# Optimization experiments

Hardware: AMD Instinct MI355X
Metric: run time of the kernel (lower is better)

The kernel has to match this reference:

```python
import jax, jax.numpy as jnp
import numpy as np

N_NODES = 500000
N_EDGES = 8000000
N_FIELDS = 4
GRAD_LIMIT = 30000.0
EPS = 1e-8


def setup_inputs() -> dict:
    key = jax.random.key(0)
    k1, k2, k3 = jax.random.split(key, 3)
    pos = jax.random.normal(k1, (N_NODES, 2), dtype=jnp.float32)
    edge_index = jax.random.randint(k2, (2, N_EDGES), 0, N_NODES, dtype=jnp.int32)
    field = jax.random.normal(k3, (N_NODES, N_FIELDS), dtype=jnp.float32)
    return {"pos": pos, "edge_index": edge_index, "field": field}


def reference(pos, edge_index, field):
    # pos: [N,2], edge_index: [2,E] int, field: [N,F]
    row, col = edge_index[0], edge_index[1]
    N = pos.shape[0]

    # Per-edge position differences (detached in the original -> stop_gradient)
    dX = jax.lax.stop_gradient(pos[col] - pos[row])  # [E,2]

    # Outer products and scatter-add into per-node 2x2 moment matrices
    M_edge = dX[:, :, None] * dX[:, None, :]                     # [E,2,2]
    M_node = jax.ops.segment_sum(M_edge, row, num_segments=N)    # [N,2,2]
    M_node = M_node + EPS * jnp.eye(2, dtype=jnp.float32)
    M_inv = jnp.linalg.inv(M_node)                               # [N,2,2]

    # All field variables at once (original loops over columns; math identical)
    du = field[col] - field[row]                                 # [E,F]
    V_edge = dX[:, :, None] * du[:, None, :]                     # [E,2,F]
    V_node = jax.ops.segment_sum(V_edge, row, num_segments=N)    # [N,2,F]

    grads = jnp.einsum('nij,njf->nif', M_inv, V_node)            # [N,2,F]
    grads = jnp.clip(grads, -GRAD_LIMIT, GRAD_LIMIT)
    # Original returns a list of F arrays of shape [N,2]; stack as [F,N,2]
    return jnp.transpose(grads, (2, 0, 1)).astype(pos.dtype)
```

## Files before the change

### kernel.cpp

```cpp
#include <hip/hip_runtime.h>
#include <hip/hip_bf16.h>


#define GRAD_LIMIT 30000.0f
#define EPS 1e-8

#define NBUCKET_MAX 1024
#define BSHIFT 9
#define BSIZE 512
#define CHUNK 8192
#define BTHREADS 512
#define PER_THREAD (CHUNK / BTHREADS)
#define CAP 10240

__global__ void pack_kernel(const float2* __restrict__ pos,
                            const float4* __restrict__ field,
                            float4* __restrict__ packed, int N) {
    int n = blockIdx.x * blockDim.x + threadIdx.x;
    if (n >= N) return;
    float2 p = pos[n];
    float4 f = field[n];
    packed[2 * n + 0] = make_float4(p.x, p.y, f.x, f.y);
    packed[2 * n + 1] = make_float4(f.z, f.w, 0.f, 0.f);
}

__global__ void __launch_bounds__(BTHREADS)
bucket_count_kernel(const int* __restrict__ rows, int* __restrict__ bucket_cnt,
                    int E, int nbuckets) {
    __shared__ int hist[NBUCKET_MAX];
    for (int i = threadIdx.x; i < nbuckets; i += blockDim.x) hist[i] = 0;
    __syncthreads();

    int base = blockIdx.x * CHUNK;
    int lim = E - base;
    if (lim > CHUNK) lim = CHUNK;
    for (int k = threadIdx.x; k < lim; k += blockDim.x) {
        int r = rows[base + k];
        atomicAdd(&hist[r >> BSHIFT], 1);
    }
    __syncthreads();
    for (int i = threadIdx.x; i < nbuckets; i += blockDim.x) {
        int c = hist[i];
        if (c) atomicAdd(&bucket_cnt[i], c);
    }
}

__global__ void bucket_scan_kernel(const int* __restrict__ bucket_cnt,
                                   int* __restrict__ bucket_start,
                                   int* __restrict__ cursor, int nb) {
    __shared__ int s[NBUCKET_MAX];
    int t = threadIdx.x;
    int v = (t < nb) ? bucket_cnt[t] : 0;
    s[t] = v;
    __syncthreads();
    for (int d = 1; d < NBUCKET_MAX; d <<= 1) {
        int x = (t >= d) ? s[t - d] : 0;
        __syncthreads();
        s[t] += x;
        __syncthreads();
    }
    if (t < nb) {
        int ex = s[t] - v;
        bucket_start[t] = ex;
        cursor[t] = ex;
    }
}

__global__ void __launch_bounds__(BTHREADS)
bucket_scatter_kernel(const int* __restrict__ rows, const int* __restrict__ cols,
                      int* __restrict__ cursor, unsigned* __restrict__ payload,
                      int E, int nbuckets) {
    __shared__ int hist[NBUCKET_MAX];
    __shared__ int lbase[NBUCKET_MAX];
    for (int i = threadIdx.x; i < nbuckets; i += blockDim.x) hist[i] = 0;
    __syncthreads();

    int base = blockIdx.x * CHUNK;
    int lim = E - base;
    if (lim > CHUNK) lim = CHUNK;

    unsigned pk[PER_THREAD];
    int bl[PER_THREAD];
#pragma unroll
    for (int k = 0; k < PER_THREAD; ++k) {
        int idx = k * BTHREADS + threadIdx.x;
        if (idx < lim) {
            int e = base + idx;
            int r = rows[e];
            int c = cols[e];
            int b = r >> BSHIFT;
            int lr = atomicAdd(&hist[b], 1);
            pk[k] = ((unsigned)(r & (BSIZE - 1)) << 19) | (unsigned)c;
            bl[k] = (b << 13) | lr;
        } else {
            bl[k] = -1;
        }
    }
    __syncthreads();
    for (int i = threadIdx.x; i < nbuckets; i += blockDim.x) {
        int c = hist[i];
        lbase[i] = c ? atomicAdd(&cursor[i], c) : 0;
    }
    __syncthreads();
#pragma unroll
    for (int k = 0; k < PER_THREAD; ++k) {
        if (bl[k] >= 0) {
            int b = bl[k] >> 13;
            int lr = bl[k] & 8191;
            payload[lbase[b] + lr] = pk[k];
        }
    }
}

__global__ void __launch_bounds__(BSIZE)
bucket_sort_accum_solve(const float4* __restrict__ packed,
                        const int* __restrict__ bucket_start,
                        const int* __restrict__ cursor,
                        const unsigned* __restrict__ payload,
                        float* __restrict__ out,
                        int N) {
    __shared__ unsigned sorted[CAP];
    __shared__ int hist[BSIZE];
    __shared__ int incl[BSIZE];
    __shared__ int cur[BSIZE];

    int t = threadIdx.x;
    int b = blockIdx.x;
    int node0 = b << BSHIFT;

    float4 ra = make_float4(0.f, 0.f, 0.f, 0.f);
    float4 rb = ra;
    if (node0 + t < N) {
        ra = packed[2 * (node0 + t) + 0];
        rb = packed[2 * (node0 + t) + 1];
    }

    float m00 = 0.f, m01 = 0.f, m11 = 0.f;
    float v00 = 0.f, v01 = 0.f, v02 = 0.f, v03 = 0.f;
    float v10 = 0.f, v11 = 0.f, v12 = 0.f, v13 = 0.f;

    int s0 = bucket_start[b];
    int s1 = cursor[b];

    for (int cstart = s0; cstart < s1; cstart += CAP) {
        int cnt = s1 - cstart;
        if (cnt > CAP) cnt = CAP;

        hist[t] = 0;
        __syncthreads();

        for (int i = t; i < cnt; i += BSIZE) {
            unsigned p = payload[cstart + i];
            atomicAdd(&hist[p >> 19], 1);
        }
        __syncthreads();

        incl[t] = hist[t];
        __syncthreads();
        for (int d = 1; d < BSIZE; d <<= 1) {
            int x = (t >= d) ? incl[t - d] : 0;
            __syncthreads();
            incl[t] += x;
            __syncthreads();
        }
        cur[t] = incl[t] - hist[t];
        __syncthreads();

        for (int i = t; i < cnt; i += BSIZE) {
            unsigned p = payload[cstart + i];
            int k = atomicAdd(&cur[p >> 19], 1);
            sorted[k] = p;
        }
        __syncthreads();

        int st = incl[t] - hist[t];
        int en = incl[t];
        for (int k = st; k < en; ++k) {
            unsigned p = sorted[k];
            int c = (int)(p & 0x7FFFFu);
            float4 ca = packed[2 * c + 0];
            float4 cb = packed[2 * c + 1];
            float dx0 = ca.x - ra.x;
            float dx1 = ca.y - ra.y;
            float du0 = ca.z - ra.z;
            float du1 = ca.w - ra.w;
            float du2 = cb.x - rb.x;
            float du3 = cb.y - rb.y;
            m00 = fmaf(dx0, dx0, m00);
            m01 = fmaf(dx0, dx1, m01);
            m11 = fmaf(dx1, dx1, m11);
            v00 = fmaf(dx0, du0, v00);
            v01 = fmaf(dx0, du1, v01);
            v02 = fmaf(dx0, du2, v02);
            v03 = fmaf(dx0, du3, v03);
            v10 = fmaf(dx1, du0, v10);
            v11 = fmaf(dx1, du1, v11);
            v12 = fmaf(dx1, du2, v12);
            v13 = fmaf(dx1, du3, v13);
        }
        __syncthreads();
    }

    int n = node0 + t;
    if (n >= N) return;
    double M00 = (double)m00 + EPS;
    double M01 = (double)m01;
    double M11 = (double)m11 + EPS;
    double inv_det = 1.0 / (M00 * M11 - M01 * M01);
    double i00 = M11 * inv_det;
    double i01 = -M01 * inv_det;
    double i11 = M00 * inv_det;

    const float vf0[4] = {v00, v01, v02, v03};
    const float vf1[4] = {v10, v11, v12, v13};
#pragma unroll
    for (int f = 0; f < 4; ++f) {
        float ga = (float)(i00 * (double)vf0[f] + i01 * (double)vf1[f]);
        float gb = (float)(i01 * (double)vf0[f] + i11 * (double)vf1[f]);
        float2 o;
        o.x = fminf(fmaxf(ga, -GRAD_LIMIT), GRAD_LIMIT);
        o.y = fminf(fmaxf(gb, -GRAD_LIMIT), GRAD_LIMIT);
        *reinterpret_cast<float2*>(out + (size_t)f * N * 2 + (size_t)n * 2) = o;
    }
}

extern "C" void kernel_launch(void* const* d_in, const int* in_sizes, int n_in,
                              void* d_out, int out_size, void* d_ws, size_t ws_size,
                              hipStream_t stream) {
    const float2* pos = (const float2*)d_in[0];
    const int* edge_index = (const int*)d_in[1];
    const float4* field = (const float4*)d_in[2];
    float* out = (float*)d_out;

    const int N = in_sizes[0] / 2;
    const int E = in_sizes[1] / 2;

    const int* rows = edge_index;
    const int* cols = edge_index + E;

    const int nbuckets = (N + BSIZE - 1) / BSIZE;
    const int nblocksE = (E + CHUNK - 1) / CHUNK;

    float4* packed = (float4*)d_ws;
    int* bucket_cnt = (int*)(packed + (size_t)2 * N);
    int* bucket_start = bucket_cnt + NBUCKET_MAX;
    int* cursor = bucket_start + NBUCKET_MAX;
    unsigned* payload = (unsigned*)(cursor + NBUCKET_MAX);

    hipMemsetAsync(bucket_cnt, 0, NBUCKET_MAX * sizeof(int), stream);
    pack_kernel<<<(N + 255) / 256, 256, 0, stream>>>(pos, field, packed, N);
    bucket_count_kernel<<<nblocksE, BTHREADS, 0, stream>>>(rows, bucket_cnt, E,
                                                           nbuckets);
    bucket_scan_kernel<<<1, NBUCKET_MAX, 0, stream>>>(bucket_cnt, bucket_start,
                                                      cursor, nbuckets);
    bucket_scatter_kernel<<<nblocksE, BTHREADS, 0, stream>>>(rows, cols, cursor,
                                                             payload, E, nbuckets);
    bucket_sort_accum_solve<<<nbuckets, BSIZE, 0, stream>>>(packed, bucket_start,
                                                            cursor, payload,
                                                            out, N);
}
```

Measured before the change: 340.6 us.

## Replace atomic bucket cursors with per-block histogram scan and register-cached payload

Edge bucketing now writes a per-block bucket histogram matrix, column-scans it and scans the bucket totals. Each scatter block then gets fixed output offsets without global atomics or a staged register pass. The sort/accumulate kernel keeps its payload entries in registers between the histogram and placement passes, so it reads payload from global memory once instead of twice. CAP shrinks to 8192, which is close to the average edges per bucket, so many buckets may need a second small chunk pass with extra barriers.

```diff
diff --git a/kernel.cpp b/kernel.cpp
--- a/kernel.cpp
+++ b/kernel.cpp
@@ -11,7 +11,9 @@
 #define CHUNK 8192
 #define BTHREADS 512
 #define PER_THREAD (CHUNK / BTHREADS)
-#define CAP 10240
+#define CHUNK_E 16384
+#define CAP 8192
+#define KC_ITERS (CAP / BSIZE)
 
 __global__ void pack_kernel(const float2* __restrict__ pos,
                             const float4* __restrict__ field,
@@ -24,20 +26,98 @@
     packed[2 * n + 1] = make_float4(f.z, f.w, 0.f, 0.f);
 }
 
+
+__global__ void __launch_bounds__(BTHREADS)
+count2_kernel(const int* __restrict__ rows, int* __restrict__ counts,
+              int E, int nbuckets) {
+    __shared__ int hist[NBUCKET_MAX];
+    for (int i = threadIdx.x; i < nbuckets; i += blockDim.x) hist[i] = 0;
+    __syncthreads();
+    int base = blockIdx.x * CHUNK_E;
+    int lim = E - base;
+    if (lim > CHUNK_E) lim = CHUNK_E;
+    for (int k = threadIdx.x; k < lim; k += blockDim.x)
+        atomicAdd(&hist[rows[base + k] >> BSHIFT], 1);
+    __syncthreads();
+    int* row = counts + (size_t)blockIdx.x * nbuckets;
+    for (int i = threadIdx.x; i < nbuckets; i += blockDim.x) row[i] = hist[i];
+}
+
+__global__ void __launch_bounds__(512)
+colscan_kernel(int* __restrict__ counts, int* __restrict__ totals,
+               int nblk, int nbuckets) {
+    __shared__ int s[512];
+    int b = blockIdx.x;
+    int t = threadIdx.x;
+    int v = (t < nblk) ? counts[(size_t)t * nbuckets + b] : 0;
+    s[t] = v;
+    __syncthreads();
+    for (int d = 1; d < 512; d <<= 1) {
+        int x = (t >= d) ? s[t - d] : 0;
+        __syncthreads();
+        s[t] += x;
+        __syncthreads();
+    }
+    if (t < nblk) counts[(size_t)t * nbuckets + b] = s[t] - v;
+    if (t == 511) totals[b] = s[511];
+}
+
+__global__ void totscan_kernel(const int* __restrict__ totals,
+                               int* __restrict__ bucket_start, int nb) {
+    __shared__ int s[1024];
+    int t = threadIdx.x;
+    int v = (t < nb) ? totals[t] : 0;
+    s[t] = v;
+    __syncthreads();
+    for (int d = 1; d < 1024; d <<= 1) {
+        int x = (t >= d) ? s[t - d] : 0;
+        __syncthreads();
+        s[t] += x;
+        __syncthreads();
+    }
+    if (t < nb) bucket_start[t] = s[t] - v;
+}
+
+__global__ void __launch_bounds__(BTHREADS)
+scatter2_kernel(const int* __restrict__ rows, const int* __restrict__ cols,
+                const int* __restrict__ bucket_start,
+                const int* __restrict__ counts,
+                unsigned* __restrict__ payload, int E, int nbuckets) {
+    __shared__ int rank[NBUCKET_MAX];
+    __shared__ int lbase[NBUCKET_MAX];
+    int blk = blockIdx.x;
+    const int* pre = counts + (size_t)blk * nbuckets;
+    for (int i = threadIdx.x; i < nbuckets; i += blockDim.x) {
+        rank[i] = 0;
+        lbase[i] = bucket_start[i] + pre[i];
+    }
+    __syncthreads();
+    int base = blk * CHUNK_E;
+    int lim = E - base;
+    if (lim > CHUNK_E) lim = CHUNK_E;
+    for (int k = threadIdx.x; k < lim; k += blockDim.x) {
+        int e = base + k;
+        int r = rows[e];
+        int c = cols[e];
+        int b = r >> BSHIFT;
+        int lr = atomicAdd(&rank[b], 1);
+        payload[lbase[b] + lr] =
+            ((unsigned)(r & (BSIZE - 1)) << 19) | (unsigned)c;
+    }
+}
+
+
 __global__ void __launch_bounds__(BTHREADS)
 bucket_count_kernel(const int* __restrict__ rows, int* __restrict__ bucket_cnt,
                     int E, int nbuckets) {
     __shared__ int hist[NBUCKET_MAX];
     for (int i = threadIdx.x; i < nbuckets; i += blockDim.x) hist[i] = 0;
     __syncthreads();
-
     int base = blockIdx.x * CHUNK;
     int lim = E - base;
     if (lim > CHUNK) lim = CHUNK;
-    for (int k = threadIdx.x; k < lim; k += blockDim.x) {
-        int r = rows[base + k];
-        atomicAdd(&hist[r >> BSHIFT], 1);
-    }
+    for (int k = threadIdx.x; k < lim; k += blockDim.x)
+        atomicAdd(&hist[rows[base + k] >> BSHIFT], 1);
     __syncthreads();
     for (int i = threadIdx.x; i < nbuckets; i += blockDim.x) {
         int c = hist[i];
@@ -74,11 +154,9 @@
     __shared__ int lbase[NBUCKET_MAX];
     for (int i = threadIdx.x; i < nbuckets; i += blockDim.x) hist[i] = 0;
     __syncthreads();
-
     int base = blockIdx.x * CHUNK;
     int lim = E - base;
     if (lim > CHUNK) lim = CHUNK;
-
     unsigned pk[PER_THREAD];
     int bl[PER_THREAD];
 #pragma unroll
@@ -115,7 +193,7 @@
 __global__ void __launch_bounds__(BSIZE)
 bucket_sort_accum_solve(const float4* __restrict__ packed,
                         const int* __restrict__ bucket_start,
-                        const int* __restrict__ cursor,
+                        const int* __restrict__ totals,
                         const unsigned* __restrict__ payload,
                         float* __restrict__ out,
                         int N) {
@@ -140,7 +218,7 @@
     float v10 = 0.f, v11 = 0.f, v12 = 0.f, v13 = 0.f;
 
     int s0 = bucket_start[b];
-    int s1 = cursor[b];
+    int s1 = s0 + totals[b];
 
     for (int cstart = s0; cstart < s1; cstart += CAP) {
         int cnt = s1 - cstart;
@@ -149,9 +227,15 @@
         hist[t] = 0;
         __syncthreads();
 
-        for (int i = t; i < cnt; i += BSIZE) {
-            unsigned p = payload[cstart + i];
-            atomicAdd(&hist[p >> 19], 1);
+        unsigned pr[KC_ITERS];
+#pragma unroll
+        for (int it = 0; it < KC_ITERS; ++it) {
+            int i = it * BSIZE + t;
+            pr[it] = 0u;
+            if (i < cnt) {
+                pr[it] = payload[cstart + i];
+                atomicAdd(&hist[pr[it] >> 19], 1);
+            }
         }
         __syncthreads();
 
@@ -166,10 +250,13 @@
         cur[t] = incl[t] - hist[t];
         __syncthreads();
 
-        for (int i = t; i < cnt; i += BSIZE) {
-            unsigned p = payload[cstart + i];
-            int k = atomicAdd(&cur[p >> 19], 1);
-            sorted[k] = p;
+#pragma unroll
+        for (int it = 0; it < KC_ITERS; ++it) {
+            int i = it * BSIZE + t;
+            if (i < cnt) {
+                int k = atomicAdd(&cur[pr[it] >> 19], 1);
+                sorted[k] = pr[it];
+            }
         }
         __syncthreads();
 
@@ -239,23 +326,53 @@
     const int* cols = edge_index + E;
 
     const int nbuckets = (N + BSIZE - 1) / BSIZE;
-    const int nblocksE = (E + CHUNK - 1) / CHUNK;
-
-    float4* packed = (float4*)d_ws;
-    int* bucket_cnt = (int*)(packed + (size_t)2 * N);
-    int* bucket_start = bucket_cnt + NBUCKET_MAX;
-    int* cursor = bucket_start + NBUCKET_MAX;
-    unsigned* payload = (unsigned*)(cursor + NBUCKET_MAX);
-
-    hipMemsetAsync(bucket_cnt, 0, NBUCKET_MAX * sizeof(int), stream);
-    pack_kernel<<<(N + 255) / 256, 256, 0, stream>>>(pos, field, packed, N);
-    bucket_count_kernel<<<nblocksE, BTHREADS, 0, stream>>>(rows, bucket_cnt, E,
-                                                           nbuckets);
-    bucket_scan_kernel<<<1, NBUCKET_MAX, 0, stream>>>(bucket_cnt, bucket_start,
-                                                      cursor, nbuckets);
-    bucket_scatter_kernel<<<nblocksE, BTHREADS, 0, stream>>>(rows, cols, cursor,
-                                                             payload, E, nbuckets);
-    bucket_sort_accum_solve<<<nbuckets, BSIZE, 0, stream>>>(packed, bucket_start,
-                                                            cursor, payload,
-                                                            out, N);
-}
+    const int nblk = (E + CHUNK_E - 1) / CHUNK_E;
+    const int nblocksF = (E + CHUNK - 1) / CHUNK;
+
+    size_t packed_bytes = (size_t)2 * N * sizeof(float4);
+    size_t counts_bytes = (size_t)nblk * nbuckets * sizeof(int);
+    size_t need_new = packed_bytes + (size_t)E * 4 + counts_bytes
+                      + (size_t)2 * NBUCKET_MAX * 4;
+
+    if (ws_size >= need_new && nblk <= 512) {
+        float4* packed = (float4*)d_ws;
+        unsigned* payload = (unsigned*)(packed + (size_t)2 * N);
+        int* counts = (int*)(payload + (size_t)E);
+        int* totals = counts + (size_t)nblk * nbuckets;
+        int* bucket_start = totals + NBUCKET_MAX;
+
+        pack_kernel<<<(N + 255) / 256, 256, 0, stream>>>(pos, field, packed, N);
+        count2_kernel<<<nblk, BTHREADS, 0, stream>>>(rows, counts, E, nbuckets);
+        colscan_kernel<<<nbuckets, 512, 0, stream>>>(counts, totals, nblk,
+                                                     nbuckets);
+        totscan_kernel<<<1, 1024, 0, stream>>>(totals, bucket_start, nbuckets);
+        scatter2_kernel<<<nblk, BTHREADS, 0, stream>>>(rows, cols, bucket_start,
+                                                       counts, payload, E,
+                                                       nbuckets);
+        bucket_sort_accum_solve<<<nbuckets, BSIZE, 0, stream>>>(packed,
+                                                                bucket_start,
+                                                                totals, payload,
+                                                                out, N);
+    } else {
+        float4* packed = (float4*)d_ws;
+        int* bucket_cnt = (int*)(packed + (size_t)2 * N);
+        int* bucket_start = bucket_cnt + NBUCKET_MAX;
+        int* cursor = bucket_start + NBUCKET_MAX;
+        unsigned* payload = (unsigned*)(cursor + NBUCKET_MAX);
+
+        hipMemsetAsync(bucket_cnt, 0, NBUCKET_MAX * sizeof(int), stream);
+        pack_kernel<<<(N + 255) / 256, 256, 0, stream>>>(pos, field, packed, N);
+        bucket_count_kernel<<<nblocksF, BTHREADS, 0, stream>>>(rows, bucket_cnt,
+                                                               E, nbuckets);
+        bucket_scan_kernel<<<1, NBUCKET_MAX, 0, stream>>>(bucket_cnt,
+                                                          bucket_start, cursor,
+                                                          nbuckets);
+        bucket_scatter_kernel<<<nblocksF, BTHREADS, 0, stream>>>(rows, cols,
+                                                                 cursor, payload,
+                                                                 E, nbuckets);
+        bucket_sort_accum_solve<<<nbuckets, BSIZE, 0, stream>>>(packed,
+                                                                bucket_start,
+                                                                bucket_cnt,
+                                                                payload, out, N);
+    }
+}
```

Result: slower. 407.4 us (+19.6%).
